# Kernel optimization log

Measured on AMD Instinct MI355X. Metric: run time of the kernel, lower is better.

## Reference

```python
import jax, jax.numpy as jnp
import numpy as np

# Dims: module math forces per-head depth D == num_points == N (see analysis).
B, H, N = 4, 8, 1024
D = N                      # q_depth = k_depth = v_depth = num_points
C_IN = 64                  # q_in = k_in = v_in
C_OUT = H * D              # q_out = k_out = v_out = 8192
SCALE = float(np.sqrt(D))


def _split_heads(t):
    # t: [B, C_OUT, N] -> view(B, H, D, N) -> permute -> [B, H, N, D]
    return t.reshape(B, H, D, N).transpose(0, 1, 3, 2)


def setup_inputs() -> dict:
    key = jax.random.key(0)
    ks = jax.random.split(key, 9)
    s = 0.02
    return {
        "coordinate": jax.random.normal(ks[0], (B, 3, N), jnp.float32),
        "x": jax.random.normal(ks[1], (B, C_IN, N, 1), jnp.float32),
        "neighbors": jax.random.normal(ks[2], (B, C_IN, N, 1), jnp.float32),
        # 1x1 Conv2d weights (out, in), no bias
        "Wq": jax.random.normal(ks[3], (C_OUT, C_IN), jnp.float32) * s,
        "Wk": jax.random.normal(ks[4], (C_OUT, C_IN), jnp.float32) * s,
        "Wv": jax.random.normal(ks[5], (C_OUT, C_IN), jnp.float32) * s,
        # nn.Linear(3, q_out) / nn.Linear(3, v_out)
        "Wlq": jax.random.normal(ks[6], (C_OUT, 3), jnp.float32) * s,
        "blq": jnp.zeros((C_OUT,), jnp.float32),
        "Wlv": jax.random.normal(ks[7], (C_OUT, 3), jnp.float32) * s,
        "blv": jnp.zeros((C_OUT,), jnp.float32),
    }


def reference(coordinate, x, neighbors, Wq, Wk, Wv, Wlq, blq, Wlv, blv):
    # Att_Score_method='dot_product', pos_method='method_ii' (hardcoded branch)
    xs = x[..., 0]           # [B, C_IN, N]  (squeeze trailing Conv2d width dim)
    ns = neighbors[..., 0]   # [B, C_IN, N]

    q = _split_heads(jnp.einsum('oc,bcn->bon', Wq, xs))  # [B,H,N,D]
    k = _split_heads(jnp.einsum('oc,bcn->bon', Wk, ns))  # [B,H,N,D]
    v = _split_heads(jnp.einsum('oc,bcn->bon', Wv, ns))  # [B,H,N,D]

    coords = coordinate.transpose(0, 2, 1)               # [B, N, 3]
    # positional encodings, split into heads: [B,H,N,D]
    pos_q = _split_heads((coords @ Wlq.T + blq).transpose(0, 2, 1))
    pos_v = _split_heads((coords @ Wlv.T + blv).transpose(0, 2, 1))

    # q_context = q @ pos_q^T ; energy = q @ k^T + q_context  -> [B,H,N,N]
    q_context = jnp.einsum('bhnd,bhmd->bhnm', q, pos_q)
    energy = jnp.einsum('bhnd,bhmd->bhnm', q, k) + q_context

    attn = jax.nn.softmax(energy / SCALE, axis=-1)       # [B,H,N,N]
    v_context = v + pos_v                                 # [B,H,N,D], D==N
    out = attn * v_context                                # elementwise combine

    # permute(0,2,1,3) -> [B,N,H,D] -> reshape [B,N,H*D] -> permute -> [B,H*D,N]
    out = out.transpose(0, 2, 1, 3).reshape(B, N, H * D).transpose(0, 2, 1)
    return out
```

## Files before the change

### kernel.cpp

```cpp
#include <hip/hip_runtime.h>

#define BB 4
#define HH 8
#define NN 1024
#define KP 96
#define LSTR 104

typedef __attribute__((ext_vector_type(8))) short short8;
typedef __attribute__((ext_vector_type(4))) short short4v;
typedef __attribute__((ext_vector_type(4))) float f32x4;

__device__ __forceinline__ short f2bf(float f){
  unsigned u = __builtin_bit_cast(unsigned, f);
  u += 0x7FFFu + ((u >> 16) & 1u);
  return (short)(u >> 16);
}

__global__ __launch_bounds__(1024) void k_prep_pt(
    const float* __restrict__ Wq, const float* __restrict__ Wk,
    const float* __restrict__ Wlq, const float* __restrict__ blq,
    short* __restrict__ PT){
  int t = threadIdx.x, c = t & 63, p = t >> 6;
  int h = blockIdx.y, kk0 = blockIdx.x * 8;
  float acc[8];
  #pragma unroll
  for (int i = 0; i < 8; ++i) acc[i] = 0.f;
  for (int dd = 0; dd < 64; ++dd){
    int o = h * 1024 + p * 64 + dd;
    float wq = Wq[o * 64 + c];
    #pragma unroll
    for (int i = 0; i < 8; ++i){
      int kk = kk0 + i;
      float bv;
      if (kk < 64)        bv = Wk[o * 64 + kk];
      else if (kk < 67)   bv = Wlq[o * 3 + (kk - 64)];
      else if (kk == 67)  bv = blq[o];
      else                bv = 0.f;
      acc[i] += wq * bv;
    }
  }
  __shared__ float red[16][64][8];
  #pragma unroll
  for (int i = 0; i < 8; ++i) red[p][c][i] = acc[i];
  __syncthreads();
  if (p == 0){
    #pragma unroll
    for (int i = 0; i < 8; ++i){
      float s = 0.f;
      for (int pp = 0; pp < 16; ++pp) s += red[pp][c][i];
      PT[(h * KP + kk0 + i) * 64 + c] = f2bf(s);
    }
  }
}

__global__ __launch_bounds__(256) void k_prep_b(
    const float* __restrict__ ns, const float* __restrict__ coord,
    short* __restrict__ Bm){
  int t = threadIdx.x;
  int b = blockIdx.y, m0 = blockIdx.x * 64;
  __shared__ float nsT[64][65];
  __shared__ float cst[3][64];
  #pragma unroll
  for (int it = 0; it < 16; ++it){
    int idx = it * 256 + t;
    int c = idx >> 6, mm = idx & 63;
    nsT[mm][c] = ns[(b * 64 + c) * NN + m0 + mm];
  }
  if (t < 192){
    int j = t >> 6, mm = t & 63;
    cst[j][mm] = coord[(b * 3 + j) * NN + m0 + mm];
  }
  __syncthreads();
  #pragma unroll
  for (int it = 0; it < 24; ++it){
    int idx = it * 256 + t;
    int mm = idx / KP, kk = idx - mm * KP;
    float v = (kk < 64) ? nsT[mm][kk]
            : (kk < 67) ? cst[kk - 64][mm]
            : (kk == 67) ? 1.f : 0.f;
    Bm[(b * NN + m0 + mm) * KP + kk] = f2bf(v);
  }
}

__global__ __launch_bounds__(256) void k_prep_v(
    const float* __restrict__ Wv, const float* __restrict__ Wlv,
    const float* __restrict__ blv, short* __restrict__ Vm){
  int t = threadIdx.x, o0 = blockIdx.x * 64;
  #pragma unroll
  for (int it = 0; it < 24; ++it){
    int idx = it * 256 + t;
    int r = idx / KP, kk = idx - r * KP;
    int o = o0 + r;
    float v = (kk < 64) ? Wv[o * 64 + kk]
            : (kk < 67) ? Wlv[o * 3 + (kk - 64)]
            : (kk == 67) ? blv[o] : 0.f;
    Vm[o * KP + kk] = f2bf(v);
  }
}

__global__ __launch_bounds__(256) void attn_main(
    const float* __restrict__ xs, const short* __restrict__ PT,
    const short* __restrict__ Bmat, const short* __restrict__ Vm,
    float* __restrict__ out){
  __shared__ short xsL[64 * 64];
  __shared__ short AL[64 * LSTR];
  __shared__ short Bst[64 * LSTR];
  __shared__ short Vst[64 * LSTR];
  const int t = threadIdx.x, w = t >> 6, lane = t & 63;
  const int q = lane >> 4, ln = lane & 15;
  const int blk = blockIdx.x, nb = blk & 15, bh = blk >> 4;
  const int b = bh >> 3, h = bh & 7;
  const int n0 = nb * 64;

  const float* xsb = xs + b * 64 * NN;
  #pragma unroll
  for (int it = 0; it < 4; ++it){
    int idx = it * 256 + t;
    int c = idx >> 4, nn4 = (idx & 15) << 2;
    f32x4 v = *(const f32x4*)(xsb + c * NN + n0 + nn4);
    short4v pk;
    #pragma unroll
    for (int j = 0; j < 4; ++j) pk[j] = f2bf(v[j]);
    *(short4v*)(&xsL[c * 64 + nn4]) = pk;
  }
  __syncthreads();

  short8 xf0, xf1;
  #pragma unroll
  for (int j = 0; j < 8; ++j){
    xf0[j] = xsL[(q * 8 + j) * 64 + w * 16 + ln];
    xf1[j] = xsL[(32 + q * 8 + j) * 64 + w * 16 + ln];
  }
  const short* PTh = PT + h * KP * 64;
  #pragma unroll
  for (int kt = 0; kt < 6; ++kt){
    short8 p0 = *(const short8*)(PTh + (kt * 16 + ln) * 64 + q * 8);
    short8 p1 = *(const short8*)(PTh + (kt * 16 + ln) * 64 + 32 + q * 8);
    f32x4 a = {0.f, 0.f, 0.f, 0.f};
    a = __builtin_amdgcn_mfma_f32_16x16x32_bf16(xf0, p0, a, 0, 0, 0);
    a = __builtin_amdgcn_mfma_f32_16x16x32_bf16(xf1, p1, a, 0, 0, 0);
    #pragma unroll
    for (int r = 0; r < 4; ++r)
      AL[(w * 16 + q * 4 + r) * LSTR + kt * 16 + ln] = f2bf(a[r]);
  }
  __syncthreads();

  short8 af[3], bn[3];
  const short* Bb = Bmat + b * NN * KP;
  #pragma unroll
  for (int s = 0; s < 3; ++s){
    af[s] = *(const short8*)(&AL[(w * 16 + ln) * LSTR + s * 32 + q * 8]);
    bn[s] = *(const short8*)(Bb + (n0 + w * 16 + ln) * KP + s * 32 + q * 8);
  }
  const float KEXP = 0.045084220f;

  float sum[4] = {0.f, 0.f, 0.f, 0.f};
  for (int mc = 0; mc < 16; ++mc){
    __syncthreads();
    #pragma unroll
    for (int it = 0; it < 3; ++it){
      int idx = it * 256 + t;
      int row = idx / 12, seg = idx - row * 12;
      *(uint4*)(&Bst[row * LSTR + seg * 8]) =
          *(const uint4*)(Bb + (mc * 64 + row) * KP + seg * 8);
    }
    __syncthreads();
    #pragma unroll
    for (int sm = 0; sm < 4; ++sm){
      f32x4 e = {0.f, 0.f, 0.f, 0.f};
      #pragma unroll
      for (int s = 0; s < 3; ++s){
        short8 bf = *(const short8*)(&Bst[(sm * 16 + ln) * LSTR + s * 32 + q * 8]);
        e = __builtin_amdgcn_mfma_f32_16x16x32_bf16(af[s], bf, e, 0, 0, 0);
      }
      #pragma unroll
      for (int r = 0; r < 4; ++r) sum[r] += __builtin_amdgcn_exp2f(e[r] * KEXP);
    }
  }
  #pragma unroll
  for (int r = 0; r < 4; ++r){
    sum[r] += __shfl_xor(sum[r], 1);
    sum[r] += __shfl_xor(sum[r], 2);
    sum[r] += __shfl_xor(sum[r], 4);
    sum[r] += __shfl_xor(sum[r], 8);
  }
  float rinv[4];
  #pragma unroll
  for (int r = 0; r < 4; ++r) rinv[r] = 1.0f / sum[r];

  float* outp = out + (size_t)bh * 1024 * 1024;
  const short* Vh = Vm + h * 1024 * KP;
  for (int dc = 0; dc < 16; ++dc){
    __syncthreads();
    #pragma unroll
    for (int it = 0; it < 3; ++it){
      int idx = it * 256 + t;
      int row = idx / 12, seg = idx - row * 12;
      *(uint4*)(&Bst[row * LSTR + seg * 8]) =
          *(const uint4*)(Bb + (dc * 64 + row) * KP + seg * 8);
      *(uint4*)(&Vst[row * LSTR + seg * 8]) =
          *(const uint4*)(Vh + (dc * 64 + row) * KP + seg * 8);
    }
    __syncthreads();
    #pragma unroll
    for (int sd = 0; sd < 4; ++sd){
      f32x4 e  = {0.f, 0.f, 0.f, 0.f};
      f32x4 vv = {0.f, 0.f, 0.f, 0.f};
      #pragma unroll
      for (int s = 0; s < 3; ++s){
        short8 bf = *(const short8*)(&Bst[(sd * 16 + ln) * LSTR + s * 32 + q * 8]);
        short8 vf = *(const short8*)(&Vst[(sd * 16 + ln) * LSTR + s * 32 + q * 8]);
        e  = __builtin_amdgcn_mfma_f32_16x16x32_bf16(af[s], bf, e, 0, 0, 0);
        vv = __builtin_amdgcn_mfma_f32_16x16x32_bf16(bn[s], vf, vv, 0, 0, 0);
      }
      f32x4 o;
      #pragma unroll
      for (int r = 0; r < 4; ++r)
        o[r] = __builtin_amdgcn_exp2f(e[r] * KEXP) * rinv[r] * vv[r];
      *(f32x4*)(outp + (dc * 64 + sd * 16 + ln) * NN + n0 + w * 16 + q * 4) = o;
    }
  }
}

extern "C" void kernel_launch(void* const* d_in, const int* in_sizes, int n_in,
                              void* d_out, int out_size, void* d_ws, size_t ws_size,
                              hipStream_t stream){
  const float* coord = (const float*)d_in[0];
  const float* x     = (const float*)d_in[1];
  const float* nbr   = (const float*)d_in[2];
  const float* Wq    = (const float*)d_in[3];
  const float* Wk    = (const float*)d_in[4];
  const float* Wv    = (const float*)d_in[5];
  const float* Wlq   = (const float*)d_in[6];
  const float* blq   = (const float*)d_in[7];
  const float* Wlv   = (const float*)d_in[8];
  const float* blv   = (const float*)d_in[9];
  float* out = (float*)d_out;

  char* ws = (char*)d_ws;
  short* PT = (short*)ws;
  short* Bm = (short*)(ws + 98304);
  short* Vm = (short*)(ws + 98304 + 786432);

  k_prep_pt<<<dim3(12, 8), 1024, 0, stream>>>(Wq, Wk, Wlq, blq, PT);
  k_prep_b <<<dim3(16, 4),  256, 0, stream>>>(nbr, coord, Bm);
  k_prep_v <<<128,          256, 0, stream>>>(Wv, Wlv, blv, Vm);
  attn_main<<<512,          256, 0, stream>>>(x, PT, Bm, Vm, out);
}
```

Baseline: 252.4 us.

## Drop LDS staging in attention loops, split prep_pt reduction with atomics

The main attention kernel no longer stages B and V tiles through shared memory with block barriers. Each wave now keeps A and B-row fragments for all 64 rows in registers, covers its own 256-column slice, and prefetches the next fragments straight from global memory one step ahead. Softmax row sums are combined across waves through a small shared buffer. The P^T prep kernel is split four ways along its reduction axis, accumulates in fp32 with atomicAdd after a memset, and attn_main converts to bf16 on load. This removes barrier and LDS traffic and exposes more parallelism in prep, at the cost of more register pressure, uncoalesced global fragment loads, and an extra memset launch.

After: 248.9 us. No clear change (-1.4%).

```diff
diff --git a/kernel.cpp b/kernel.cpp
--- a/kernel.cpp
+++ b/kernel.cpp
@@ -1,7 +1,5 @@
 #include <hip/hip_runtime.h>
 
-#define BB 4
-#define HH 8
 #define NN 1024
 #define KP 96
 #define LSTR 104
@@ -19,36 +17,37 @@
 __global__ __launch_bounds__(1024) void k_prep_pt(
     const float* __restrict__ Wq, const float* __restrict__ Wk,
     const float* __restrict__ Wlq, const float* __restrict__ blq,
-    short* __restrict__ PT){
+    float* __restrict__ PTf){
   int t = threadIdx.x, c = t & 63, p = t >> 6;
-  int h = blockIdx.y, kk0 = blockIdx.x * 8;
+  int h = blockIdx.y, kk0 = blockIdx.x * 8, dz = blockIdx.z;
   float acc[8];
   #pragma unroll
   for (int i = 0; i < 8; ++i) acc[i] = 0.f;
-  for (int dd = 0; dd < 64; ++dd){
-    int o = h * 1024 + p * 64 + dd;
+  #pragma unroll
+  for (int i = 0; i < 16; ++i){
+    int o = h * 1024 + p * 64 + dz * 16 + i;
     float wq = Wq[o * 64 + c];
     #pragma unroll
-    for (int i = 0; i < 8; ++i){
-      int kk = kk0 + i;
+    for (int j = 0; j < 8; ++j){
+      int kk = kk0 + j;
       float bv;
       if (kk < 64)        bv = Wk[o * 64 + kk];
       else if (kk < 67)   bv = Wlq[o * 3 + (kk - 64)];
       else if (kk == 67)  bv = blq[o];
       else                bv = 0.f;
-      acc[i] += wq * bv;
+      acc[j] += wq * bv;
     }
   }
   __shared__ float red[16][64][8];
   #pragma unroll
-  for (int i = 0; i < 8; ++i) red[p][c][i] = acc[i];
+  for (int j = 0; j < 8; ++j) red[p][c][j] = acc[j];
   __syncthreads();
   if (p == 0){
     #pragma unroll
-    for (int i = 0; i < 8; ++i){
+    for (int j = 0; j < 8; ++j){
       float s = 0.f;
-      for (int pp = 0; pp < 16; ++pp) s += red[pp][c][i];
-      PT[(h * KP + kk0 + i) * 64 + c] = f2bf(s);
+      for (int pp = 0; pp < 16; ++pp) s += red[pp][c][j];
+      atomicAdd(&PTf[(h * KP + kk0 + j) * 64 + c], s);
     }
   }
 }
@@ -99,13 +98,12 @@
 }
 
 __global__ __launch_bounds__(256) void attn_main(
-    const float* __restrict__ xs, const short* __restrict__ PT,
+    const float* __restrict__ xs, const float* __restrict__ PTf,
     const short* __restrict__ Bmat, const short* __restrict__ Vm,
     float* __restrict__ out){
   __shared__ short xsL[64 * 64];
   __shared__ short AL[64 * LSTR];
-  __shared__ short Bst[64 * LSTR];
-  __shared__ short Vst[64 * LSTR];
+  __shared__ float redS[64 * 4];
   const int t = threadIdx.x, w = t >> 6, lane = t & 63;
   const int q = lane >> 4, ln = lane & 15;
   const int blk = blockIdx.x, nb = blk & 15, bh = blk >> 4;
@@ -131,11 +129,20 @@
     xf0[j] = xsL[(q * 8 + j) * 64 + w * 16 + ln];
     xf1[j] = xsL[(32 + q * 8 + j) * 64 + w * 16 + ln];
   }
-  const short* PTh = PT + h * KP * 64;
+  const float* PTh = PTf + h * KP * 64;
   #pragma unroll
   for (int kt = 0; kt < 6; ++kt){
-    short8 p0 = *(const short8*)(PTh + (kt * 16 + ln) * 64 + q * 8);
-    short8 p1 = *(const short8*)(PTh + (kt * 16 + ln) * 64 + 32 + q * 8);
+    const float* pr = PTh + (kt * 16 + ln) * 64;
+    f32x4 pa = *(const f32x4*)(pr + q * 8);
+    f32x4 pb = *(const f32x4*)(pr + q * 8 + 4);
+    f32x4 pc = *(const f32x4*)(pr + 32 + q * 8);
+    f32x4 pd = *(const f32x4*)(pr + 32 + q * 8 + 4);
+    short8 p0, p1;
+    #pragma unroll
+    for (int j = 0; j < 4; ++j){
+      p0[j] = f2bf(pa[j]); p0[4 + j] = f2bf(pb[j]);
+      p1[j] = f2bf(pc[j]); p1[4 + j] = f2bf(pd[j]);
+    }
     f32x4 a = {0.f, 0.f, 0.f, 0.f};
     a = __builtin_amdgcn_mfma_f32_16x16x32_bf16(xf0, p0, a, 0, 0, 0);
     a = __builtin_amdgcn_mfma_f32_16x16x32_bf16(xf1, p1, a, 0, 0, 0);
@@ -145,80 +152,117 @@
   }
   __syncthreads();
 
-  short8 af[3], bn[3];
+  short8 af[4][3], bn[4][3];
   const short* Bb = Bmat + b * NN * KP;
   #pragma unroll
-  for (int s = 0; s < 3; ++s){
-    af[s] = *(const short8*)(&AL[(w * 16 + ln) * LSTR + s * 32 + q * 8]);
-    bn[s] = *(const short8*)(Bb + (n0 + w * 16 + ln) * KP + s * 32 + q * 8);
+  for (int rf = 0; rf < 4; ++rf){
+    #pragma unroll
+    for (int s = 0; s < 3; ++s){
+      af[rf][s] = *(const short8*)(&AL[(rf * 16 + ln) * LSTR + s * 32 + q * 8]);
+      bn[rf][s] = *(const short8*)(Bb + (n0 + rf * 16 + ln) * KP + s * 32 + q * 8);
+    }
   }
   const float KEXP = 0.045084220f;
 
-  float sum[4] = {0.f, 0.f, 0.f, 0.f};
-  for (int mc = 0; mc < 16; ++mc){
-    __syncthreads();
-    #pragma unroll
-    for (int it = 0; it < 3; ++it){
-      int idx = it * 256 + t;
-      int row = idx / 12, seg = idx - row * 12;
-      *(uint4*)(&Bst[row * LSTR + seg * 8]) =
-          *(const uint4*)(Bb + (mc * 64 + row) * KP + seg * 8);
-    }
-    __syncthreads();
-    #pragma unroll
-    for (int sm = 0; sm < 4; ++sm){
+  float sum[4][4];
+  #pragma unroll
+  for (int rf = 0; rf < 4; ++rf)
+    #pragma unroll
+    for (int r = 0; r < 4; ++r) sum[rf][r] = 0.f;
+
+  short8 bf0, bf1, bf2;
+  {
+    const short* bp = Bb + (w * 256 + ln) * KP + q * 8;
+    bf0 = *(const short8*)(bp);
+    bf1 = *(const short8*)(bp + 32);
+    bf2 = *(const short8*)(bp + 64);
+  }
+  for (int ms = 0; ms < 16; ++ms){
+    short8 nb0, nb1, nb2;
+    {
+      int msn = (ms + 1) & 15;
+      const short* bp = Bb + (w * 256 + msn * 16 + ln) * KP + q * 8;
+      nb0 = *(const short8*)(bp);
+      nb1 = *(const short8*)(bp + 32);
+      nb2 = *(const short8*)(bp + 64);
+    }
+    #pragma unroll
+    for (int rf = 0; rf < 4; ++rf){
       f32x4 e = {0.f, 0.f, 0.f, 0.f};
+      e = __builtin_amdgcn_mfma_f32_16x16x32_bf16(af[rf][0], bf0, e, 0, 0, 0);
+      e = __builtin_amdgcn_mfma_f32_16x16x32_bf16(af[rf][1], bf1, e, 0, 0, 0);
+      e = __builtin_amdgcn_mfma_f32_16x16x32_bf16(af[rf][2], bf2, e, 0, 0, 0);
       #pragma unroll
-      for (int s = 0; s < 3; ++s){
-        short8 bf = *(const short8*)(&Bst[(sm * 16 + ln) * LSTR + s * 32 + q * 8]);
-        e = __builtin_amdgcn_mfma_f32_16x16x32_bf16(af[s], bf, e, 0, 0, 0);
-      }
+      for (int r = 0; r < 4; ++r)
+        sum[rf][r] += __builtin_amdgcn_exp2f(e[r] * KEXP);
+    }
+    bf0 = nb0; bf1 = nb1; bf2 = nb2;
+  }
+  #pragma unroll
+  for (int rf = 0; rf < 4; ++rf){
+    #pragma unroll
+    for (int r = 0; r < 4; ++r){
+      float s = sum[rf][r];
+      s += __shfl_xor(s, 1); s += __shfl_xor(s, 2);
+      s += __shfl_xor(s, 4); s += __shfl_xor(s, 8);
+      sum[rf][r] = s;
+    }
+  }
+  if (ln == 0){
+    #pragma unroll
+    for (int rf = 0; rf < 4; ++rf)
       #pragma unroll
-      for (int r = 0; r < 4; ++r) sum[r] += __builtin_amdgcn_exp2f(e[r] * KEXP);
-    }
-  }
-  #pragma unroll
-  for (int r = 0; r < 4; ++r){
-    sum[r] += __shfl_xor(sum[r], 1);
-    sum[r] += __shfl_xor(sum[r], 2);
-    sum[r] += __shfl_xor(sum[r], 4);
-    sum[r] += __shfl_xor(sum[r], 8);
-  }
-  float rinv[4];
-  #pragma unroll
-  for (int r = 0; r < 4; ++r) rinv[r] = 1.0f / sum[r];
-
-  float* outp = out + (size_t)bh * 1024 * 1024;
+      for (int r = 0; r < 4; ++r)
+        redS[(rf * 16 + q * 4 + r) * 4 + w] = sum[rf][r];
+  }
+  __syncthreads();
+  float rinv[4][4];
+  #pragma unroll
+  for (int rf = 0; rf < 4; ++rf){
+    #pragma unroll
+    for (int r = 0; r < 4; ++r){
+      f32x4 v4 = *(const f32x4*)(&redS[(rf * 16 + q * 4 + r) * 4]);
+      rinv[rf][r] = 1.0f / (v4[0] + v4[1] + v4[2] + v4[3]);
+    }
+  }
+
+  float* outp = out + (size_t)bh * (1024 * 1024);
   const short* Vh = Vm + h * 1024 * KP;
-  for (int dc = 0; dc < 16; ++dc){
-    __syncthreads();
-    #pragma unroll
-    for (int it = 0; it < 3; ++it){
-      int idx = it * 256 + t;
-      int row = idx / 12, seg = idx - row * 12;
-      *(uint4*)(&Bst[row * LSTR + seg * 8]) =
-          *(const uint4*)(Bb + (dc * 64 + row) * KP + seg * 8);
-      *(uint4*)(&Vst[row * LSTR + seg * 8]) =
-          *(const uint4*)(Vh + (dc * 64 + row) * KP + seg * 8);
-    }
-    __syncthreads();
-    #pragma unroll
-    for (int sd = 0; sd < 4; ++sd){
+  short8 vf0, vf1, vf2;
+  {
+    const short* bp = Bb + (w * 256 + ln) * KP + q * 8;
+    const short* vp = Vh + (w * 256 + ln) * KP + q * 8;
+    bf0 = *(const short8*)(bp); bf1 = *(const short8*)(bp + 32); bf2 = *(const short8*)(bp + 64);
+    vf0 = *(const short8*)(vp); vf1 = *(const short8*)(vp + 32); vf2 = *(const short8*)(vp + 64);
+  }
+  for (int ds = 0; ds < 16; ++ds){
+    int d0 = w * 256 + ds * 16;
+    short8 nb0, nb1, nb2, nv0, nv1, nv2;
+    {
+      int dsn = (ds + 1) & 15;
+      const short* bp = Bb + (w * 256 + dsn * 16 + ln) * KP + q * 8;
+      const short* vp = Vh + (w * 256 + dsn * 16 + ln) * KP + q * 8;
+      nb0 = *(const short8*)(bp); nb1 = *(const short8*)(bp + 32); nb2 = *(const short8*)(bp + 64);
+      nv0 = *(const short8*)(vp); nv1 = *(const short8*)(vp + 32); nv2 = *(const short8*)(vp + 64);
+    }
+    #pragma unroll
+    for (int rf = 0; rf < 4; ++rf){
       f32x4 e  = {0.f, 0.f, 0.f, 0.f};
       f32x4 vv = {0.f, 0.f, 0.f, 0.f};
-      #pragma unroll
-      for (int s = 0; s < 3; ++s){
-        short8 bf = *(const short8*)(&Bst[(sd * 16 + ln) * LSTR + s * 32 + q * 8]);
-        short8 vf = *(const short8*)(&Vst[(sd * 16 + ln) * LSTR + s * 32 + q * 8]);
-        e  = __builtin_amdgcn_mfma_f32_16x16x32_bf16(af[s], bf, e, 0, 0, 0);
-        vv = __builtin_amdgcn_mfma_f32_16x16x32_bf16(bn[s], vf, vv, 0, 0, 0);
-      }
+      e  = __builtin_amdgcn_mfma_f32_16x16x32_bf16(af[rf][0], bf0, e, 0, 0, 0);
+      e  = __builtin_amdgcn_mfma_f32_16x16x32_bf16(af[rf][1], bf1, e, 0, 0, 0);
+      e  = __builtin_amdgcn_mfma_f32_16x16x32_bf16(af[rf][2], bf2, e, 0, 0, 0);
+      vv = __builtin_amdgcn_mfma_f32_16x16x32_bf16(bn[rf][0], vf0, vv, 0, 0, 0);
+      vv = __builtin_amdgcn_mfma_f32_16x16x32_bf16(bn[rf][1], vf1, vv, 0, 0, 0);
+      vv = __builtin_amdgcn_mfma_f32_16x16x32_bf16(bn[rf][2], vf2, vv, 0, 0, 0);
       f32x4 o;
       #pragma unroll
       for (int r = 0; r < 4; ++r)
-        o[r] = __builtin_amdgcn_exp2f(e[r] * KEXP) * rinv[r] * vv[r];
-      *(f32x4*)(outp + (dc * 64 + sd * 16 + ln) * NN + n0 + w * 16 + q * 4) = o;
-    }
+        o[r] = __builtin_amdgcn_exp2f(e[r] * KEXP) * rinv[rf][r] * vv[r];
+      *(f32x4*)(outp + (d0 + ln) * NN + n0 + rf * 16 + q * 4) = o;
+    }
+    bf0 = nb0; bf1 = nb1; bf2 = nb2;
+    vf0 = nv0; vf1 = nv1; vf2 = nv2;
   }
 }
 
@@ -238,12 +282,13 @@
   float* out = (float*)d_out;
 
   char* ws = (char*)d_ws;
-  short* PT = (short*)ws;
-  short* Bm = (short*)(ws + 98304);
-  short* Vm = (short*)(ws + 98304 + 786432);
-
-  k_prep_pt<<<dim3(12, 8), 1024, 0, stream>>>(Wq, Wk, Wlq, blq, PT);
-  k_prep_b <<<dim3(16, 4),  256, 0, stream>>>(nbr, coord, Bm);
-  k_prep_v <<<128,          256, 0, stream>>>(Wv, Wlv, blv, Vm);
-  attn_main<<<512,          256, 0, stream>>>(x, PT, Bm, Vm, out);
-}
+  float* PTf = (float*)ws;
+  short* Bm  = (short*)(ws + 196608);
+  short* Vm  = (short*)(ws + 196608 + 786432);
+
+  hipMemsetAsync(PTf, 0, 196608, stream);
+  k_prep_pt<<<dim3(12, 8, 4), 1024, 0, stream>>>(Wq, Wk, Wlq, blq, PTf);
+  k_prep_b <<<dim3(16, 4),     256, 0, stream>>>(nbr, coord, Bm);
+  k_prep_v <<<128,             256, 0, stream>>>(Wv, Wlv, blv, Vm);
+  attn_main<<<512,             256, 0, stream>>>(x, PTf, Bm, Vm, out);
+}
```

## Merge prep kernels and cache softmax probabilities in registers across passes

Applied to the files above, without the earlier changes.

Fuses the three preprocessing kernels into one launch with block-index dispatch. In the main kernel, blocks now cover 32 query rows and each wave owns a quarter of the key/depth range. Exp values from the sum pass are kept as packed bf16 in registers, so the second pass no longer recomputes the QK MFMAs and exps. LDS staging and its barriers are replaced by direct global fragment loads. The costs are much higher register pressure from the 64-word probability cache, bf16 rounding of the probabilities, and a cross-wave LDS reduction for the row sums.

New measurement: 431.6 us. 71.0% more time.

```diff
diff --git a/kernel.cpp b/kernel.cpp
--- a/kernel.cpp
+++ b/kernel.cpp
@@ -1,7 +1,5 @@
 #include <hip/hip_runtime.h>
 
-#define BB 4
-#define HH 8
 #define NN 1024
 #define KP 96
 #define LSTR 104
@@ -16,85 +14,81 @@
   return (short)(u >> 16);
 }
 
-__global__ __launch_bounds__(1024) void k_prep_pt(
+__global__ __launch_bounds__(256) void prep_all(
     const float* __restrict__ Wq, const float* __restrict__ Wk,
     const float* __restrict__ Wlq, const float* __restrict__ blq,
-    short* __restrict__ PT){
-  int t = threadIdx.x, c = t & 63, p = t >> 6;
-  int h = blockIdx.y, kk0 = blockIdx.x * 8;
-  float acc[8];
-  #pragma unroll
-  for (int i = 0; i < 8; ++i) acc[i] = 0.f;
-  for (int dd = 0; dd < 64; ++dd){
-    int o = h * 1024 + p * 64 + dd;
-    float wq = Wq[o * 64 + c];
-    #pragma unroll
-    for (int i = 0; i < 8; ++i){
-      int kk = kk0 + i;
-      float bv;
-      if (kk < 64)        bv = Wk[o * 64 + kk];
-      else if (kk < 67)   bv = Wlq[o * 3 + (kk - 64)];
-      else if (kk == 67)  bv = blq[o];
-      else                bv = 0.f;
-      acc[i] += wq * bv;
-    }
-  }
-  __shared__ float red[16][64][8];
-  #pragma unroll
-  for (int i = 0; i < 8; ++i) red[p][c][i] = acc[i];
-  __syncthreads();
-  if (p == 0){
-    #pragma unroll
-    for (int i = 0; i < 8; ++i){
-      float s = 0.f;
-      for (int pp = 0; pp < 16; ++pp) s += red[pp][c][i];
-      PT[(h * KP + kk0 + i) * 64 + c] = f2bf(s);
-    }
-  }
-}
-
-__global__ __launch_bounds__(256) void k_prep_b(
-    const float* __restrict__ ns, const float* __restrict__ coord,
-    short* __restrict__ Bm){
-  int t = threadIdx.x;
-  int b = blockIdx.y, m0 = blockIdx.x * 64;
-  __shared__ float nsT[64][65];
-  __shared__ float cst[3][64];
-  #pragma unroll
-  for (int it = 0; it < 16; ++it){
-    int idx = it * 256 + t;
-    int c = idx >> 6, mm = idx & 63;
-    nsT[mm][c] = ns[(b * 64 + c) * NN + m0 + mm];
-  }
-  if (t < 192){
-    int j = t >> 6, mm = t & 63;
-    cst[j][mm] = coord[(b * 3 + j) * NN + m0 + mm];
-  }
-  __syncthreads();
-  #pragma unroll
-  for (int it = 0; it < 24; ++it){
-    int idx = it * 256 + t;
-    int mm = idx / KP, kk = idx - mm * KP;
-    float v = (kk < 64) ? nsT[mm][kk]
-            : (kk < 67) ? cst[kk - 64][mm]
-            : (kk == 67) ? 1.f : 0.f;
-    Bm[(b * NN + m0 + mm) * KP + kk] = f2bf(v);
-  }
-}
-
-__global__ __launch_bounds__(256) void k_prep_v(
     const float* __restrict__ Wv, const float* __restrict__ Wlv,
-    const float* __restrict__ blv, short* __restrict__ Vm){
-  int t = threadIdx.x, o0 = blockIdx.x * 64;
-  #pragma unroll
-  for (int it = 0; it < 24; ++it){
-    int idx = it * 256 + t;
-    int r = idx / KP, kk = idx - r * KP;
-    int o = o0 + r;
-    float v = (kk < 64) ? Wv[o * 64 + kk]
-            : (kk < 67) ? Wlv[o * 3 + (kk - 64)]
-            : (kk == 67) ? blv[o] : 0.f;
-    Vm[o * KP + kk] = f2bf(v);
+    const float* __restrict__ blv, const float* __restrict__ ns,
+    const float* __restrict__ coord,
+    short* __restrict__ PT, short* __restrict__ Bm, short* __restrict__ Vm){
+  const int bz = blockIdx.x, t = threadIdx.x;
+  if (bz < 32){
+    __shared__ float red[4][64][24];
+    int h = bz >> 2, kq = bz & 3;
+    int c = t & 63, p = t >> 6;
+    float acc[24];
+    #pragma unroll
+    for (int j = 0; j < 24; ++j) acc[j] = 0.f;
+    for (int i = 0; i < 256; ++i){
+      int o = h * 1024 + p * 256 + i;
+      float wq = Wq[o * 64 + c];
+      #pragma unroll
+      for (int j = 0; j < 24; ++j){
+        int kk = kq * 24 + j;
+        float bv;
+        if (kk < 64)        bv = Wk[o * 64 + kk];
+        else if (kk < 67)   bv = Wlq[o * 3 + (kk - 64)];
+        else if (kk == 67)  bv = blq[o];
+        else                bv = 0.f;
+        acc[j] += wq * bv;
+      }
+    }
+    #pragma unroll
+    for (int j = 0; j < 24; ++j) red[p][c][j] = acc[j];
+    __syncthreads();
+    if (p == 0){
+      #pragma unroll
+      for (int j = 0; j < 24; ++j){
+        float s = red[0][c][j] + red[1][c][j] + red[2][c][j] + red[3][c][j];
+        PT[(h * KP + kq * 24 + j) * 64 + c] = f2bf(s);
+      }
+    }
+  } else if (bz < 96){
+    __shared__ float nsT[64][65];
+    __shared__ float cst[3][64];
+    int idx0 = bz - 32, b = idx0 >> 4, m0 = (idx0 & 15) * 64;
+    #pragma unroll
+    for (int it = 0; it < 16; ++it){
+      int idx = it * 256 + t;
+      int c = idx >> 6, mm = idx & 63;
+      nsT[mm][c] = ns[(b * 64 + c) * NN + m0 + mm];
+    }
+    if (t < 192){
+      int j = t >> 6, mm = t & 63;
+      cst[j][mm] = coord[(b * 3 + j) * NN + m0 + mm];
+    }
+    __syncthreads();
+    #pragma unroll
+    for (int it = 0; it < 24; ++it){
+      int idx = it * 256 + t;
+      int mm = idx / KP, kk = idx - mm * KP;
+      float v = (kk < 64) ? nsT[mm][kk]
+              : (kk < 67) ? cst[kk - 64][mm]
+              : (kk == 67) ? 1.f : 0.f;
+      Bm[(b * NN + m0 + mm) * KP + kk] = f2bf(v);
+    }
+  } else {
+    int o0 = (bz - 96) * 64;
+    #pragma unroll
+    for (int it = 0; it < 24; ++it){
+      int idx = it * 256 + t;
+      int r = idx / KP, kk = idx - r * KP;
+      int o = o0 + r;
+      float v = (kk < 64) ? Wv[o * 64 + kk]
+              : (kk < 67) ? Wlv[o * 3 + (kk - 64)]
+              : (kk == 67) ? blv[o] : 0.f;
+      Vm[o * KP + kk] = f2bf(v);
+    }
   }
 }
 
@@ -102,122 +96,136 @@
     const float* __restrict__ xs, const short* __restrict__ PT,
     const short* __restrict__ Bmat, const short* __restrict__ Vm,
     float* __restrict__ out){
-  __shared__ short xsL[64 * 64];
-  __shared__ short AL[64 * LSTR];
-  __shared__ short Bst[64 * LSTR];
-  __shared__ short Vst[64 * LSTR];
+  __shared__ short xsL[64 * 32];
+  __shared__ short AL[32 * LSTR];
+  __shared__ float redS[32 * 4];
   const int t = threadIdx.x, w = t >> 6, lane = t & 63;
   const int q = lane >> 4, ln = lane & 15;
-  const int blk = blockIdx.x, nb = blk & 15, bh = blk >> 4;
+  const int blk = blockIdx.x, nb = blk & 31, bh = blk >> 5;
   const int b = bh >> 3, h = bh & 7;
-  const int n0 = nb * 64;
+  const int n0 = nb * 32;
 
   const float* xsb = xs + b * 64 * NN;
   #pragma unroll
-  for (int it = 0; it < 4; ++it){
+  for (int it = 0; it < 2; ++it){
     int idx = it * 256 + t;
-    int c = idx >> 4, nn4 = (idx & 15) << 2;
+    int c = idx >> 3, nn4 = (idx & 7) << 2;
     f32x4 v = *(const f32x4*)(xsb + c * NN + n0 + nn4);
     short4v pk;
     #pragma unroll
     for (int j = 0; j < 4; ++j) pk[j] = f2bf(v[j]);
-    *(short4v*)(&xsL[c * 64 + nn4]) = pk;
+    *(short4v*)(&xsL[c * 32 + nn4]) = pk;
   }
   __syncthreads();
 
+  const int rh = w & 1;
   short8 xf0, xf1;
   #pragma unroll
   for (int j = 0; j < 8; ++j){
-    xf0[j] = xsL[(q * 8 + j) * 64 + w * 16 + ln];
-    xf1[j] = xsL[(32 + q * 8 + j) * 64 + w * 16 + ln];
+    xf0[j] = xsL[(q * 8 + j) * 32 + rh * 16 + ln];
+    xf1[j] = xsL[(32 + q * 8 + j) * 32 + rh * 16 + ln];
   }
   const short* PTh = PT + h * KP * 64;
   #pragma unroll
-  for (int kt = 0; kt < 6; ++kt){
-    short8 p0 = *(const short8*)(PTh + (kt * 16 + ln) * 64 + q * 8);
-    short8 p1 = *(const short8*)(PTh + (kt * 16 + ln) * 64 + 32 + q * 8);
+  for (int jt = 0; jt < 3; ++jt){
+    int kt = (w >> 1) + 2 * jt;
+    const short* pr = PTh + (kt * 16 + ln) * 64;
+    short8 p0 = *(const short8*)(pr + q * 8);
+    short8 p1 = *(const short8*)(pr + 32 + q * 8);
     f32x4 a = {0.f, 0.f, 0.f, 0.f};
     a = __builtin_amdgcn_mfma_f32_16x16x32_bf16(xf0, p0, a, 0, 0, 0);
     a = __builtin_amdgcn_mfma_f32_16x16x32_bf16(xf1, p1, a, 0, 0, 0);
     #pragma unroll
     for (int r = 0; r < 4; ++r)
-      AL[(w * 16 + q * 4 + r) * LSTR + kt * 16 + ln] = f2bf(a[r]);
+      AL[(rh * 16 + q * 4 + r) * LSTR + kt * 16 + ln] = f2bf(a[r]);
   }
   __syncthreads();
 
-  short8 af[3], bn[3];
+  short8 af[2][3], bn[2][3];
   const short* Bb = Bmat + b * NN * KP;
   #pragma unroll
-  for (int s = 0; s < 3; ++s){
-    af[s] = *(const short8*)(&AL[(w * 16 + ln) * LSTR + s * 32 + q * 8]);
-    bn[s] = *(const short8*)(Bb + (n0 + w * 16 + ln) * KP + s * 32 + q * 8);
+  for (int rf = 0; rf < 2; ++rf){
+    #pragma unroll
+    for (int s = 0; s < 3; ++s){
+      af[rf][s] = *(const short8*)(&AL[(rf * 16 + ln) * LSTR + s * 32 + q * 8]);
+      bn[rf][s] = *(const short8*)(Bb + (n0 + rf * 16 + ln) * KP + s * 32 + q * 8);
+    }
   }
   const float KEXP = 0.045084220f;
 
-  float sum[4] = {0.f, 0.f, 0.f, 0.f};
-  for (int mc = 0; mc < 16; ++mc){
-    __syncthreads();
-    #pragma unroll
-    for (int it = 0; it < 3; ++it){
-      int idx = it * 256 + t;
-      int row = idx / 12, seg = idx - row * 12;
-      *(uint4*)(&Bst[row * LSTR + seg * 8]) =
-          *(const uint4*)(Bb + (mc * 64 + row) * KP + seg * 8);
-    }
-    __syncthreads();
-    #pragma unroll
-    for (int sm = 0; sm < 4; ++sm){
+  float sum[2][4];
+  #pragma unroll
+  for (int rf = 0; rf < 2; ++rf)
+    #pragma unroll
+    for (int r = 0; r < 4; ++r) sum[rf][r] = 0.f;
+  unsigned pw[2][4][8];
+
+  #pragma unroll
+  for (int ms = 0; ms < 16; ++ms){
+    const short* bp = Bb + (w * 256 + ms * 16 + ln) * KP + q * 8;
+    short8 bf0 = *(const short8*)(bp);
+    short8 bf1 = *(const short8*)(bp + 32);
+    short8 bf2 = *(const short8*)(bp + 64);
+    #pragma unroll
+    for (int rf = 0; rf < 2; ++rf){
       f32x4 e = {0.f, 0.f, 0.f, 0.f};
-      #pragma unroll
-      for (int s = 0; s < 3; ++s){
-        short8 bf = *(const short8*)(&Bst[(sm * 16 + ln) * LSTR + s * 32 + q * 8]);
-        e = __builtin_amdgcn_mfma_f32_16x16x32_bf16(af[s], bf, e, 0, 0, 0);
-      }
-      #pragma unroll
-      for (int r = 0; r < 4; ++r) sum[r] += __builtin_amdgcn_exp2f(e[r] * KEXP);
-    }
-  }
-  #pragma unroll
-  for (int r = 0; r < 4; ++r){
-    sum[r] += __shfl_xor(sum[r], 1);
-    sum[r] += __shfl_xor(sum[r], 2);
-    sum[r] += __shfl_xor(sum[r], 4);
-    sum[r] += __shfl_xor(sum[r], 8);
-  }
-  float rinv[4];
-  #pragma unroll
-  for (int r = 0; r < 4; ++r) rinv[r] = 1.0f / sum[r];
-
-  float* outp = out + (size_t)bh * 1024 * 1024;
+      e = __builtin_amdgcn_mfma_f32_16x16x32_bf16(af[rf][0], bf0, e, 0, 0, 0);
+      e = __builtin_amdgcn_mfma_f32_16x16x32_bf16(af[rf][1], bf1, e, 0, 0, 0);
+      e = __builtin_amdgcn_mfma_f32_16x16x32_bf16(af[rf][2], bf2, e, 0, 0, 0);
+      #pragma unroll
+      for (int r = 0; r < 4; ++r){
+        float pe = __builtin_amdgcn_exp2f(e[r] * KEXP);
+        sum[rf][r] += pe;
+        unsigned hb = (unsigned)(unsigned short)f2bf(pe);
+        if (ms & 1) pw[rf][r][ms >> 1] |= hb << 16;
+        else        pw[rf][r][ms >> 1]  = hb;
+      }
+    }
+  }
+  #pragma unroll
+  for (int rf = 0; rf < 2; ++rf){
+    #pragma unroll
+    for (int r = 0; r < 4; ++r){
+      float s = sum[rf][r];
+      s += __shfl_xor(s, 1); s += __shfl_xor(s, 2);
+      s += __shfl_xor(s, 4); s += __shfl_xor(s, 8);
+      if (ln == 0) redS[(rf * 16 + q * 4 + r) * 4 + w] = s;
+    }
+  }
+  __syncthreads();
+  float rinv[2][4];
+  #pragma unroll
+  for (int rf = 0; rf < 2; ++rf){
+    #pragma unroll
+    for (int r = 0; r < 4; ++r){
+      f32x4 v4 = *(const f32x4*)(&redS[(rf * 16 + q * 4 + r) * 4]);
+      rinv[rf][r] = 1.0f / (v4[0] + v4[1] + v4[2] + v4[3]);
+    }
+  }
+
+  float* outp = out + (size_t)bh * (1024 * 1024);
   const short* Vh = Vm + h * 1024 * KP;
-  for (int dc = 0; dc < 16; ++dc){
-    __syncthreads();
-    #pragma unroll
-    for (int it = 0; it < 3; ++it){
-      int idx = it * 256 + t;
-      int row = idx / 12, seg = idx - row * 12;
-      *(uint4*)(&Bst[row * LSTR + seg * 8]) =
-          *(const uint4*)(Bb + (dc * 64 + row) * KP + seg * 8);
-      *(uint4*)(&Vst[row * LSTR + seg * 8]) =
-          *(const uint4*)(Vh + (dc * 64 + row) * KP + seg * 8);
-    }
-    __syncthreads();
-    #pragma unroll
-    for (int sd = 0; sd < 4; ++sd){
-      f32x4 e  = {0.f, 0.f, 0.f, 0.f};
+  #pragma unroll
+  for (int ds = 0; ds < 16; ++ds){
+    const short* vp = Vh + (w * 256 + ds * 16 + ln) * KP + q * 8;
+    short8 vf0 = *(const short8*)(vp);
+    short8 vf1 = *(const short8*)(vp + 32);
+    short8 vf2 = *(const short8*)(vp + 64);
+    #pragma unroll
+    for (int rf = 0; rf < 2; ++rf){
       f32x4 vv = {0.f, 0.f, 0.f, 0.f};
-      #pragma unroll
-      for (int s = 0; s < 3; ++s){
-        short8 bf = *(const short8*)(&Bst[(sd * 16 + ln) * LSTR + s * 32 + q * 8]);
-        short8 vf = *(const short8*)(&Vst[(sd * 16 + ln) * LSTR + s * 32 + q * 8]);
-        e  = __builtin_amdgcn_mfma_f32_16x16x32_bf16(af[s], bf, e, 0, 0, 0);
-        vv = __builtin_amdgcn_mfma_f32_16x16x32_bf16(bn[s], vf, vv, 0, 0, 0);
-      }
+      vv = __builtin_amdgcn_mfma_f32_16x16x32_bf16(bn[rf][0], vf0, vv, 0, 0, 0);
+      vv = __builtin_amdgcn_mfma_f32_16x16x32_bf16(bn[rf][1], vf1, vv, 0, 0, 0);
+      vv = __builtin_amdgcn_mfma_f32_16x16x32_bf16(bn[rf][2], vf2, vv, 0, 0, 0);
       f32x4 o;
       #pragma unroll
-      for (int r = 0; r < 4; ++r)
-        o[r] = __builtin_amdgcn_exp2f(e[r] * KEXP) * rinv[r] * vv[r];
-      *(f32x4*)(outp + (dc * 64 + sd * 16 + ln) * NN + n0 + w * 16 + q * 4) = o;
+      for (int r = 0; r < 4; ++r){
+        unsigned u = pw[rf][r][ds >> 1];
+        float pf = __builtin_bit_cast(float,
+            (ds & 1) ? (u & 0xFFFF0000u) : (u << 16));
+        o[r] = pf * rinv[rf][r] * vv[r];
+      }
+      *(f32x4*)(outp + (w * 256 + ds * 16 + ln) * NN + n0 + rf * 16 + q * 4) = o;
     }
   }
 }
@@ -242,8 +250,7 @@
   short* Bm = (short*)(ws + 98304);
   short* Vm = (short*)(ws + 98304 + 786432);
 
-  k_prep_pt<<<dim3(12, 8), 1024, 0, stream>>>(Wq, Wk, Wlq, blq, PT);
-  k_prep_b <<<dim3(16, 4),  256, 0, stream>>>(nbr, coord, Bm);
-  k_prep_v <<<128,          256, 0, stream>>>(Wv, Wlv, blv, Vm);
-  attn_main<<<512,          256, 0, stream>>>(x, PT, Bm, Vm, out);
-}
+  prep_all<<<224,  256, 0, stream>>>(Wq, Wk, Wlq, blq, Wv, Wlv, blv, nbr, coord,
+                                     PT, Bm, Vm);
+  attn_main<<<1024, 256, 0, stream>>>(x, PT, Bm, Vm, out);
+}
```
